# Optimization experiments

Measured on AMD Instinct MI355X. Metric: run time of the kernel, lower is better.

The kernel has to match this reference:

```python
import jax, jax.numpy as jnp
import numpy as np

B, F, D_IN, H, HEADS, NC = 2048, 64, 32, 128, 4, 16
EPG = 128            # random intra-graph edges per graph
N = B * F            # 131072 nodes
E = B * EPG          # 262144 edges (self-loops added in reference, like PyG GATConv)
LRELU_ATT = 0.2      # PyG GATConv negative_slope
LRELU_CLS = 0.01     # nn.LeakyReLU default


def setup_inputs() -> dict:
    key = jax.random.key(0)
    ks = jax.random.split(key, 24)
    emb = jax.random.normal(ks[0], (B, F, D_IN), jnp.float32)
    # per-graph random connectivity, offset so graphs are disjoint
    src_l = jax.random.randint(ks[1], (B, EPG), 0, F)
    tgt_l = jax.random.randint(ks[2], (B, EPG), 0, F)
    off = (jnp.arange(B) * F)[:, None]
    edge_index = jnp.stack([(src_l + off).reshape(-1), (tgt_l + off).reshape(-1)]).astype(jnp.int32)
    batch_idx = jnp.repeat(jnp.arange(B), F).astype(jnp.int32)
    s = 0.05
    return {
        'emb': emb, 'edge_index': edge_index, 'batch_idx': batch_idx,
        # fused aligner (single unique dim 32)
        'W_align': s * jax.random.normal(ks[3], (D_IN, H), jnp.float32),
        'b_align': jnp.zeros((H,), jnp.float32),
        'gate_logits': jnp.full((F,), 2.2, jnp.float32),
        # GATConv 1: in=H, out=H per head, heads=4, concat
        'W1': s * jax.random.normal(ks[4], (H, HEADS * H), jnp.float32),
        'a_src1': s * jax.random.normal(ks[5], (HEADS, H), jnp.float32),
        'a_dst1': s * jax.random.normal(ks[6], (HEADS, H), jnp.float32),
        'b1': jnp.zeros((HEADS * H,), jnp.float32),
        # GATConv 2: in=HEADS*H, out=H, heads=1, concat=False
        'W2': s * jax.random.normal(ks[7], (HEADS * H, H), jnp.float32),
        'a_src2': s * jax.random.normal(ks[8], (1, H), jnp.float32),
        'a_dst2': s * jax.random.normal(ks[9], (1, H), jnp.float32),
        'b2': jnp.zeros((H,), jnp.float32),
        # classifier MLP
        'Wc1': s * jax.random.normal(ks[10], (H, H // 2), jnp.float32),
        'bc1': jnp.zeros((H // 2,), jnp.float32),
        'Wc2': s * jax.random.normal(ks[11], (H // 2, NC), jnp.float32),
        'bc2': jnp.zeros((NC,), jnp.float32),
    }


def gat_layer(x, src, tgt, W, a_src, a_dst, b, concat):
    heads, dout = a_src.shape
    n = x.shape[0]
    h = (x @ W).reshape(n, heads, dout)                       # [N,h,d]
    e = jax.nn.leaky_relu(jnp.einsum('nhd,hd->nh', h, a_src)[src]
                          + jnp.einsum('nhd,hd->nh', h, a_dst)[tgt], LRELU_ATT)  # [E,h]
    m = jax.ops.segment_max(e, tgt, num_segments=n)           # segment softmax over in-neighbors
    p = jnp.exp(e - m[tgt])
    ssum = jax.ops.segment_sum(p, tgt, num_segments=n)
    alpha = p / (ssum[tgt] + 1e-16)
    out = jax.ops.segment_sum(h[src] * alpha[:, :, None], tgt, num_segments=n)
    out = out.reshape(n, heads * dout) if concat else out.mean(axis=1)
    return out + b


def reference(emb, edge_index, batch_idx, W_align, b_align, gate_logits,
              W1, a_src1, a_dst1, b1, W2, a_src2, a_dst2, b2, Wc1, bc1, Wc2, bc2):
    n = emb.shape[0] * emb.shape[1]
    aligned = emb @ W_align + b_align                         # fused align: [B,F,H]
    gate = jax.nn.sigmoid(gate_logits)                        # [F]
    x = (aligned * gate[None, :, None]).reshape(n, -1)        # gated node features [N,H]
    # add self-loops (GATConv default), eval mode -> dropout is identity
    loops = jnp.arange(n, dtype=edge_index.dtype)
    src = jnp.concatenate([edge_index[0], loops])
    tgt = jnp.concatenate([edge_index[1], loops])
    x = gat_layer(x, src, tgt, W1, a_src1, a_dst1, b1, True)  # [N, 4*H]
    x = jax.nn.elu(x)
    x = gat_layer(x, src, tgt, W2, a_src2, a_dst2, b2, False) # [N, H]
    gsum = jax.ops.segment_sum(x, batch_idx, num_segments=B)  # global_mean_pool
    cnt = jax.ops.segment_sum(jnp.ones((n, 1), x.dtype), batch_idx, num_segments=B)
    g = gsum / cnt                                            # [B, H]
    hc = jax.nn.leaky_relu(g @ Wc1 + bc1, LRELU_CLS)
    logits = hc @ Wc2 + bc2                                   # [B, NC]
    return logits, gate
```

## Files before the change

### kernel.cpp

```cpp
#include <hip/hip_runtime.h>
#include <math.h>

#define BLK 256

constexpr int Bg    = 2048;
constexpr int Fn    = 64;
constexpr int DIN   = 32;
constexpr int Hd    = 128;
constexpr int HEADS = 4;
constexpr int NC    = 16;
constexpr int EPG   = 128;
constexpr int Etot  = Bg * EPG;
constexpr int W1C   = HEADS * Hd;
constexpr int NSTR  = 68;
constexpr int EROW  = 132;
constexpr int PROW  = 68;
constexpr int NE    = EPG + Fn;

typedef __attribute__((ext_vector_type(8))) __bf16 bf16x8;
typedef __attribute__((ext_vector_type(4))) __bf16 bf16x4;
typedef __attribute__((ext_vector_type(4))) float  f32x4;

__device__ __align__(16) __bf16 g_wcombT[W1C * DIN];
__device__ float g_c1[W1C];
__device__ float g_c1s[16];
__device__ __align__(16) __bf16 g_w1F[HEADS*8*64*8];
__device__ __align__(16) __bf16 g_w2F[HEADS*4*8*64*8];
__device__ __align__(16) __bf16 g_wscF[HEADS*4*64*8];
__device__ __align__(16) __bf16 g_bs1F[64*8];

__global__ __launch_bounds__(BLK) void prep1(
    const float* __restrict__ Wa, const float* __restrict__ ba,
    const float* __restrict__ W1)
{
  __shared__ float WaS[DIN * Hd];
  const int tid = threadIdx.x;
  for (int i = tid; i < DIN * Hd; i += BLK) {
    int k = i >> 7, m = i & 127;
    WaS[m * DIN + k] = Wa[i];
  }
  __syncthreads();

  int i = blockIdx.x * BLK + tid;
  if (i < DIN * W1C) {
    int k = i & 31, n = i >> 5;
    float a0 = 0.f, a1 = 0.f, a2 = 0.f, a3 = 0.f;
    #pragma unroll
    for (int m = 0; m < Hd; m += 4) {
      a0 += WaS[(m  )*DIN + k] * W1[(m  )*W1C + n];
      a1 += WaS[(m+1)*DIN + k] * W1[(m+1)*W1C + n];
      a2 += WaS[(m+2)*DIN + k] * W1[(m+2)*W1C + n];
      a3 += WaS[(m+3)*DIN + k] * W1[(m+3)*W1C + n];
    }
    g_wcombT[i] = (__bf16)(a0 + a1 + a2 + a3);
  } else if (i < DIN*W1C + W1C) {
    int n = i - DIN*W1C;
    float a0 = 0.f, a1 = 0.f, a2 = 0.f, a3 = 0.f;
    #pragma unroll
    for (int m = 0; m < Hd; m += 4) {
      a0 += ba[m  ] * W1[(m  )*W1C + n];
      a1 += ba[m+1] * W1[(m+1)*W1C + n];
      a2 += ba[m+2] * W1[(m+2)*W1C + n];
      a3 += ba[m+3] * W1[(m+3)*W1C + n];
    }
    g_c1[n] = a0 + a1 + a2 + a3;
  }
}

constexpr int R_W2F  = 65536;
constexpr int R_W1F  = 16384;
constexpr int R_WSCZ = 8192;
constexpr int R_WSCD = 4096;
constexpr int R_BS1Z = 512;
constexpr int R_BS1D = 1024;
constexpr int R_C1S  = 128;
constexpr int B0 = R_W2F;
constexpr int B1 = B0 + R_W1F;
constexpr int B2 = B1 + R_WSCZ;
constexpr int B3 = B2 + R_WSCD;
constexpr int B4 = B3 + R_BS1Z;
constexpr int B5 = B4 + R_BS1D;
constexpr int P2_TOT = B5 + R_C1S;

__global__ __launch_bounds__(BLK) void prep2(
    const float* __restrict__ W2,
    const float* __restrict__ as1, const float* __restrict__ ad1,
    const float* __restrict__ as2, const float* __restrict__ ad2)
{
  int i = blockIdx.x * BLK + threadIdx.x;
  if (i < B0) {
    int k = i >> 7, n = i & 127;
    int hh = k >> 7, Ks = (k >> 5) & 3, q = (k >> 3) & 3, j = k & 7;
    int Nt = n >> 4, l = n & 15;
    int idx = (((hh*4 + Ks)*8 + Nt)*64 + (q*16 + l))*8 + j;
    g_w2F[idx] = (__bf16)W2[i];
  } else if (i < B1) {
    int j = i - B0;
    int jj = j & 7, lane = (j >> 3) & 63, T = j >> 9;
    int hh = T >> 3, Nt = T & 7;
    int q = lane >> 4, l = lane & 15;
    g_w1F[j] = g_wcombT[(hh*Hd + Nt*16 + l)*DIN + q*8 + jj];
  } else if (i < B2) {
    int j = i - B1;
    int lane = (j >> 3) & 63, c = lane & 15;
    if (c >= 2) g_wscF[j] = (__bf16)0.f;
  } else if (i < B3) {
    int j = i - B2;
    int p = j & 3, c = (j >> 2) & 1, k = j >> 3;
    const float* av = c ? ad2 : as2;
    float a0 = 0.f, a1 = 0.f, a2 = 0.f, a3 = 0.f;
    #pragma unroll
    for (int q = 0; q < 32; q += 4) {
      int f = p*32 + q;
      a0 += W2[(size_t)k*Hd + f    ] * av[f    ];
      a1 += W2[(size_t)k*Hd + f + 1] * av[f + 1];
      a2 += W2[(size_t)k*Hd + f + 2] * av[f + 2];
      a3 += W2[(size_t)k*Hd + f + 3] * av[f + 3];
    }
    float a = a0 + a1 + a2 + a3;
    a += __shfl_xor(a, 1);
    a += __shfl_xor(a, 2);
    if (p == 0) {
      int T = k >> 5, q2 = (k >> 3) & 3, jj = k & 7;
      g_wscF[(T*64 + q2*16 + c)*8 + jj] = (__bf16)a;
    }
  } else if (i < B4) {
    int j = i - B3;
    int lane = j >> 3, c = lane & 15;
    if (c >= 8) g_bs1F[j] = (__bf16)0.f;
  } else if (i < B5) {
    int j = i - B4;
    int p = j & 3, c = (j >> 2) & 7, kk = j >> 5;
    int h = c >> 1;
    const float* av = (c & 1) ? (ad1 + h*Hd) : (as1 + h*Hd);
    float a0 = 0.f, a1 = 0.f, a2 = 0.f, a3 = 0.f;
    #pragma unroll
    for (int q = 0; q < 32; q += 4) {
      int f = p*32 + q;
      a0 += (float)g_wcombT[(h*Hd + f    )*DIN + kk] * av[f    ];
      a1 += (float)g_wcombT[(h*Hd + f + 1)*DIN + kk] * av[f + 1];
      a2 += (float)g_wcombT[(h*Hd + f + 2)*DIN + kk] * av[f + 2];
      a3 += (float)g_wcombT[(h*Hd + f + 3)*DIN + kk] * av[f + 3];
    }
    float a = a0 + a1 + a2 + a3;
    a += __shfl_xor(a, 1);
    a += __shfl_xor(a, 2);
    if (p == 0) {
      int q2 = kk >> 3, jj = kk & 7;
      g_bs1F[(q2*16 + c)*8 + jj] = (__bf16)a;
    }
  } else if (i < P2_TOT) {
    int j = i - B5;
    int p = j & 7, c = j >> 3;
    float a = 0.f;
    if (c < 8) {
      int h = c >> 1;
      const float* av = (c & 1) ? (ad1 + h*Hd) : (as1 + h*Hd);
      #pragma unroll
      for (int q = 0; q < 16; ++q) {
        int f = p*16 + q;
        a += g_c1[h*Hd + f] * av[f];
      }
    }
    a += __shfl_xor(a, 1);
    a += __shfl_xor(a, 2);
    a += __shfl_xor(a, 4);
    if (p == 0) g_c1s[c] = a;
  }
}

#define SUMP(buf, t) ((float*)((char*)&Pbf[buf][(t)*PROW] + 128))
#define RCP(x) __builtin_amdgcn_rcpf(x)
__global__ __launch_bounds__(BLK, 3) void gat_main(
    const float* __restrict__ emb, const int* __restrict__ ei,
    const float* __restrict__ gate_logits,
    const float* __restrict__ b1, const float* __restrict__ b2,
    const float* __restrict__ Wc1, const float* __restrict__ bc1,
    const float* __restrict__ Wc2, const float* __restrict__ bc2,
    float* __restrict__ out)
{
  __shared__ __align__(16) __bf16 hT[Hd * NSTR];
  __shared__ __align__(16) __bf16 eluS[Fn * EROW];
  __shared__ __align__(16) __bf16 Pbf[2][Fn * PROW];
  __shared__ float sS1s[HEADS][Fn], sS1d[HEADS][Fn];

  unsigned* cells = (unsigned*)eluS;
  float*   gateS  = (float*)(eluS + 8192);
  float*   sSrc   = (float*)&Pbf[1][0];
  float*   sDst   = sSrc + Fn;
  __bf16*  wS     = (__bf16*)(sDst + Fn);
  float*   gpool  = (float*)(wS + Fn);
  float*   hcS    = gpool + Hd;

  const int b    = blockIdx.x;
  const int tid  = threadIdx.x;
  const int lane = tid & 63;
  const int wv   = tid >> 6;
  const int quad = lane >> 4;
  const int l15  = lane & 15;
  const int nodeBase = wv * 16;
  const int m0   = wv * 32;
  const int base = b * Fn;

  const f32x4 zero4 = {0.f, 0.f, 0.f, 0.f};

  int es = 0, et = 0, ecell = 0;
  if (tid < NE) {
    if (tid < EPG) {
      es = ei[(size_t)b*EPG + tid] - base;
      et = ei[(size_t)Etot + (size_t)b*EPG + tid] - base;
    } else {
      es = et = tid - EPG;
    }
    ecell = et * Fn + es;
  }
  {
    float4* c4 = (float4*)cells;
    const float4 z4 = {0.f,0.f,0.f,0.f};
    c4[tid] = z4; c4[tid + 256] = z4; c4[tid + 512] = z4; c4[tid + 768] = z4;
  }
  {
    float4* p4 = (float4*)&Pbf[0][0];
    const float4 z4 = {0.f,0.f,0.f,0.f};
    #pragma unroll
    for (int k = 0; k < 4; ++k) p4[tid + k*BLK] = z4;
    if (tid < 64) p4[1024 + tid] = z4;
  }
  if (tid < Fn) {
    float g = 1.f / (1.f + expf(-gate_logits[tid]));
    gateS[tid] = g;
    if (b == 0) out[Bg*NC + tid] = g;
  }
  float4 e0, e1;
  {
    const float* ar = emb + ((size_t)base + nodeBase + l15) * DIN + quad * 8;
    e0 = *(const float4*)ar;
    e1 = *(const float4*)(ar + 4);
  }
  __syncthreads();

  bool rep = false;
  if (tid < NE) rep = (atomicAdd(&cells[ecell], 1u) == 0u);

  float gq[4];
  #pragma unroll
  for (int r = 0; r < 4; ++r) gq[r] = gateS[nodeBase + quad*4 + r];

  bf16x8 Af;
  {
    const float gl = gateS[nodeBase + l15];
    Af[0]=(__bf16)(e0.x*gl); Af[1]=(__bf16)(e0.y*gl); Af[2]=(__bf16)(e0.z*gl); Af[3]=(__bf16)(e0.w*gl);
    Af[4]=(__bf16)(e1.x*gl); Af[5]=(__bf16)(e1.y*gl); Af[6]=(__bf16)(e1.z*gl); Af[7]=(__bf16)(e1.w*gl);
  }
  {
    bf16x8 Bs = *(const bf16x8*)(g_bs1F + lane*8);
    f32x4 ds = __builtin_amdgcn_mfma_f32_16x16x32_bf16(Af, Bs, zero4, 0, 0, 0);
    if (l15 < 8) {
      const float cc = g_c1s[l15];
      const int h = l15 >> 1;
      float* dstArr = (l15 & 1) ? &sS1d[h][0] : &sS1s[h][0];
      #pragma unroll
      for (int r = 0; r < 4; ++r) {
        int m = nodeBase + quad*4 + r;
        dstArr[m] = ds[r] + gq[r] * cc;
      }
    }
  }
  #pragma unroll
  for (int Nt = 0; Nt < 8; ++Nt) {
    const int n = Nt*16 + l15;
    bf16x8 Bf = *(const bf16x8*)(g_w1F + ((0*8 + Nt)*64 + lane)*8);
    f32x4 d = __builtin_amdgcn_mfma_f32_16x16x32_bf16(Af, Bf, zero4, 0, 0, 0);
    const float c1v = g_c1[0*Hd + n];
    bf16x4 hw;
    #pragma unroll
    for (int r = 0; r < 4; ++r) hw[r] = (__bf16)(d[r] + c1v * gq[r]);
    *(bf16x4*)(hT + n*NSTR + nodeBase + quad*4) = hw;
  }
  __syncthreads();

  float fm = 0.f;
  if (tid < NE && rep) {
    fm = (float)cells[ecell];
    float e = sS1s[0][es] + sS1d[0][et];
    e = (e > 0.f) ? e : 0.2f * e;
    float pe = fm * __expf(e);
    Pbf[0][et*PROW + es] = (__bf16)pe;
    atomicAdd(SUMP(0, et), pe);
  }
  __syncthreads();

  f32x4 acc[8];
  #pragma unroll
  for (int i = 0; i < 8; ++i) acc[i] = zero4;
  f32x4 accS = zero4;

  #pragma unroll 1
  for (int hh = 0; hh < HEADS; ++hh) {
    const int cur = hh & 1;
    {
      bf16x8 Ac[2][2];
      #pragma unroll
      for (int Mi = 0; Mi < 2; ++Mi)
        #pragma unroll
        for (int Ks = 0; Ks < 2; ++Ks)
          Ac[Mi][Ks] = *(const bf16x8*)(hT + (m0 + Mi*16 + l15)*NSTR + Ks*32 + quad*8);
      float4 b1v[2];
      #pragma unroll
      for (int Mi = 0; Mi < 2; ++Mi)
        b1v[Mi] = *(const float4*)&b1[hh*Hd + m0 + Mi*16 + quad*4];
      #pragma unroll
      for (int Nt = 0; Nt < 4; ++Nt) {
        bf16x8 B0f = *(const bf16x8*)(Pbf[cur] + (Nt*16 + l15)*PROW + quad*8);
        bf16x8 B1f = *(const bf16x8*)(Pbf[cur] + (Nt*16 + l15)*PROW + 32 + quad*8);
        const int t = Nt*16 + l15;
        const float si = RCP(*SUMP(cur, t) + 1e-16f);
        #pragma unroll
        for (int Mi = 0; Mi < 2; ++Mi) {
          f32x4 d = __builtin_amdgcn_mfma_f32_16x16x32_bf16(Ac[Mi][0], B0f, zero4, 0, 0, 0);
          d = __builtin_amdgcn_mfma_f32_16x16x32_bf16(Ac[Mi][1], B1f, d, 0, 0, 0);
          bf16x4 w;
          #pragma unroll
          for (int r = 0; r < 4; ++r) {
            float hv = d[r]*si + b1v[Mi][r];
            hv = (hv > 0.f) ? hv : (__expf(hv) - 1.f);
            w[r] = (__bf16)hv;
          }
          *(bf16x4*)(eluS + t*EROW + m0 + Mi*16 + quad*4) = w;
        }
      }
    }
    if (hh >= 1) {
      float4* p4 = (float4*)&Pbf[(hh+1)&1][0];
      const float4 z4 = {0.f,0.f,0.f,0.f};
      p4[tid] = z4; p4[tid + 256] = z4;
      if (tid < 32) p4[tid + 512] = z4;
    }
    __syncthreads();

    #pragma unroll
    for (int Ks = 0; Ks < 4; ++Ks) {
      bf16x8 A2 = *(const bf16x8*)(eluS + (nodeBase + l15)*EROW + Ks*32 + quad*8);
      #pragma unroll
      for (int Nt = 0; Nt < 8; ++Nt) {
        bf16x8 B2 = *(const bf16x8*)(g_w2F + (((hh*4 + Ks)*8 + Nt)*64 + lane)*8);
        acc[Nt] = __builtin_amdgcn_mfma_f32_16x16x32_bf16(A2, B2, acc[Nt], 0, 0, 0);
      }
      bf16x8 Bs2 = *(const bf16x8*)(g_wscF + ((hh*4 + Ks)*64 + lane)*8);
      accS = __builtin_amdgcn_mfma_f32_16x16x32_bf16(A2, Bs2, accS, 0, 0, 0);
    }
    if (hh < 3) {
      #pragma unroll
      for (int Nt = 0; Nt < 8; ++Nt) {
        const int n = Nt*16 + l15;
        bf16x8 Bf = *(const bf16x8*)(g_w1F + (((hh+1)*8 + Nt)*64 + lane)*8);
        f32x4 d = __builtin_amdgcn_mfma_f32_16x16x32_bf16(Af, Bf, zero4, 0, 0, 0);
        const float c1v = g_c1[(hh+1)*Hd + n];
        bf16x4 hw;
        #pragma unroll
        for (int r = 0; r < 4; ++r) hw[r] = (__bf16)(d[r] + c1v * gq[r]);
        *(bf16x4*)(hT + n*NSTR + nodeBase + quad*4) = hw;
      }
      if (tid < NE && rep) {
        float e = sS1s[hh+1][es] + sS1d[hh+1][et];
        e = (e > 0.f) ? e : 0.2f * e;
        float pe = fm * __expf(e);
        Pbf[(hh+1)&1][et*PROW + es] = (__bf16)pe;
        atomicAdd(SUMP((hh+1)&1, et), pe);
      }
    } else {
      #pragma unroll
      for (int Nt = 0; Nt < 8; ++Nt) {
        const int n = Nt*16 + l15;
        bf16x4 hw;
        #pragma unroll
        for (int r = 0; r < 4; ++r) hw[r] = (__bf16)acc[Nt][r];
        *(bf16x4*)(hT + n*NSTR + nodeBase + quad*4) = hw;
      }
      if (l15 == 0) {
        #pragma unroll
        for (int r = 0; r < 4; ++r) sSrc[nodeBase + quad*4 + r] = accS[r];
      } else if (l15 == 1) {
        #pragma unroll
        for (int r = 0; r < 4; ++r) sDst[nodeBase + quad*4 + r] = accS[r];
      }
    }
    __syncthreads();
  }

  if (tid < NE && rep) {
    float e = sSrc[es] + sDst[et];
    e = (e > 0.f) ? e : 0.2f * e;
    float pe = fm * __expf(e);
    Pbf[0][et*PROW + es] = (__bf16)pe;
    atomicAdd(SUMP(0, et), pe);
  }
  __syncthreads();

  {
    const int s_ = tid >> 2, part = tid & 3;
    float a = 0.f;
    #pragma unroll
    for (int q = 0; q < 16; ++q) {
      const int t = part*16 + q;
      a += RCP(*SUMP(0, t) + 1e-16f) * (float)Pbf[0][t*PROW + s_];
    }
    a += __shfl_xor(a, 1);
    a += __shfl_xor(a, 2);
    if (part == 0) wS[s_] = (__bf16)(a * (1.f/64.f));
  }
  __syncthreads();

  {
    #pragma unroll
    for (int Mi = 0; Mi < 2; ++Mi) {
      f32x4 d = zero4;
      #pragma unroll
      for (int Ks = 0; Ks < 2; ++Ks) {
        bf16x8 A = *(const bf16x8*)(hT + (m0 + Mi*16 + l15)*NSTR + Ks*32 + quad*8);
        bf16x8 Bw = *(const bf16x8*)(wS + Ks*32 + quad*8);
        d = __builtin_amdgcn_mfma_f32_16x16x32_bf16(A, Bw, d, 0, 0, 0);
      }
      if (l15 == 0) {
        #pragma unroll
        for (int r = 0; r < 4; ++r) {
          const int f = m0 + Mi*16 + quad*4 + r;
          gpool[f] = d[r] + b2[f];
        }
      }
    }
  }
  __syncthreads();

  {
    const int c = tid >> 2, p = tid & 3;
    float a = 0.f;
    #pragma unroll
    for (int i = 0; i < 32; ++i) {
      const int k = p*32 + i;
      a += gpool[k] * Wc1[k*Fn + c];
    }
    a += __shfl_xor(a, 1);
    a += __shfl_xor(a, 2);
    if (p == 0) {
      a += bc1[c];
      hcS[c] = (a > 0.f) ? a : 0.01f * a;
    }
  }
  __syncthreads();

  {
    const int c = tid >> 4, p = tid & 15;
    float a = 0.f;
    #pragma unroll
    for (int i = 0; i < 4; ++i) {
      const int k = p*4 + i;
      a += hcS[k] * Wc2[k*NC + c];
    }
    a += __shfl_xor(a, 1);
    a += __shfl_xor(a, 2);
    a += __shfl_xor(a, 4);
    a += __shfl_xor(a, 8);
    if (p == 0) out[b*NC + c] = a + bc2[c];
  }
}
#undef SUMP
#undef RCP

extern "C" void kernel_launch(void* const* d_in, const int* in_sizes, int n_in,
                              void* d_out, int out_size, void* d_ws, size_t ws_size,
                              hipStream_t stream) {
  const float* emb = (const float*)d_in[0];
  const int*   ei  = (const int*)  d_in[1];
  const float* Wa  = (const float*)d_in[3];
  const float* ba  = (const float*)d_in[4];
  const float* gl  = (const float*)d_in[5];
  const float* W1  = (const float*)d_in[6];
  const float* as1 = (const float*)d_in[7];
  const float* ad1 = (const float*)d_in[8];
  const float* b1  = (const float*)d_in[9];
  const float* W2  = (const float*)d_in[10];
  const float* as2 = (const float*)d_in[11];
  const float* ad2 = (const float*)d_in[12];
  const float* b2  = (const float*)d_in[13];
  const float* Wc1 = (const float*)d_in[14];
  const float* bc1 = (const float*)d_in[15];
  const float* Wc2 = (const float*)d_in[16];
  const float* bc2 = (const float*)d_in[17];
  float* out = (float*)d_out;

  const int prep1N = DIN*W1C + W1C;
  hipLaunchKernelGGL(prep1, dim3((prep1N + BLK - 1)/BLK), dim3(BLK), 0, stream,
                     Wa, ba, W1);
  hipLaunchKernelGGL(prep2, dim3((P2_TOT + BLK - 1)/BLK), dim3(BLK), 0, stream,
                     W2, as1, ad1, as2, ad2);
  hipLaunchKernelGGL(gat_main, dim3(Bg), dim3(BLK), 0, stream,
                     emb, ei, gl, b1, b2, Wc1, bc1, Wc2, bc2, out);
}
```

Baseline: 189.7 us.

## Double block size to eight waves and split feature tiles across wave halves

The main kernel now launches 512-thread blocks. Each of the four node groups is handled by two waves, and those two waves split the output-feature N tiles of the W1 and W2 matmuls between them. The aggregation M tiles and the pooling and classifier reductions are redistributed over all eight waves. The goal is more waves per CU and shorter per-wave serial MFMA chains under the same per-block LDS footprint. The trade-offs are duplicated emb loads, extra shuffle steps, and an aggressive launch-bounds hint that may cap registers and cause spills.

```diff
diff --git a/kernel.cpp b/kernel.cpp
--- a/kernel.cpp
+++ b/kernel.cpp
@@ -2,6 +2,7 @@
 #include <math.h>
 
 #define BLK 256
+#define MBLK 512
 
 constexpr int Bg    = 2048;
 constexpr int Fn    = 64;
@@ -171,7 +172,7 @@
 
 #define SUMP(buf, t) ((float*)((char*)&Pbf[buf][(t)*PROW] + 128))
 #define RCP(x) __builtin_amdgcn_rcpf(x)
-__global__ __launch_bounds__(BLK, 3) void gat_main(
+__global__ __launch_bounds__(MBLK, 6) void gat_main(
     const float* __restrict__ emb, const int* __restrict__ ei,
     const float* __restrict__ gate_logits,
     const float* __restrict__ b1, const float* __restrict__ b2,
@@ -196,10 +197,12 @@
   const int tid  = threadIdx.x;
   const int lane = tid & 63;
   const int wv   = tid >> 6;
+  const int ng   = wv & 3;
+  const int nh   = wv >> 2;
   const int quad = lane >> 4;
   const int l15  = lane & 15;
-  const int nodeBase = wv * 16;
-  const int m0   = wv * 32;
+  const int nodeBase = ng * 16;
+  const int m0   = wv * 16;
   const int base = b * Fn;
 
   const f32x4 zero4 = {0.f, 0.f, 0.f, 0.f};
@@ -217,13 +220,12 @@
   {
     float4* c4 = (float4*)cells;
     const float4 z4 = {0.f,0.f,0.f,0.f};
-    c4[tid] = z4; c4[tid + 256] = z4; c4[tid + 512] = z4; c4[tid + 768] = z4;
+    c4[tid] = z4; c4[tid + 512] = z4;
   }
   {
     float4* p4 = (float4*)&Pbf[0][0];
     const float4 z4 = {0.f,0.f,0.f,0.f};
-    #pragma unroll
-    for (int k = 0; k < 4; ++k) p4[tid + k*BLK] = z4;
+    p4[tid] = z4; p4[tid + 512] = z4;
     if (tid < 64) p4[1024 + tid] = z4;
   }
   if (tid < Fn) {
@@ -252,7 +254,7 @@
     Af[0]=(__bf16)(e0.x*gl); Af[1]=(__bf16)(e0.y*gl); Af[2]=(__bf16)(e0.z*gl); Af[3]=(__bf16)(e0.w*gl);
     Af[4]=(__bf16)(e1.x*gl); Af[5]=(__bf16)(e1.y*gl); Af[6]=(__bf16)(e1.z*gl); Af[7]=(__bf16)(e1.w*gl);
   }
-  {
+  if (nh == 0) {
     bf16x8 Bs = *(const bf16x8*)(g_bs1F + lane*8);
     f32x4 ds = __builtin_amdgcn_mfma_f32_16x16x32_bf16(Af, Bs, zero4, 0, 0, 0);
     if (l15 < 8) {
@@ -267,9 +269,10 @@
     }
   }
   #pragma unroll
-  for (int Nt = 0; Nt < 8; ++Nt) {
-    const int n = Nt*16 + l15;
-    bf16x8 Bf = *(const bf16x8*)(g_w1F + ((0*8 + Nt)*64 + lane)*8);
+  for (int Nt = 0; Nt < 4; ++Nt) {
+    const int Ntg = nh*4 + Nt;
+    const int n = Ntg*16 + l15;
+    bf16x8 Bf = *(const bf16x8*)(g_w1F + ((0*8 + Ntg)*64 + lane)*8);
     f32x4 d = __builtin_amdgcn_mfma_f32_16x16x32_bf16(Af, Bf, zero4, 0, 0, 0);
     const float c1v = g_c1[0*Hd + n];
     bf16x4 hw;
@@ -290,51 +293,43 @@
   }
   __syncthreads();
 
-  f32x4 acc[8];
+  f32x4 acc[4];
   #pragma unroll
-  for (int i = 0; i < 8; ++i) acc[i] = zero4;
+  for (int i = 0; i < 4; ++i) acc[i] = zero4;
   f32x4 accS = zero4;
 
   #pragma unroll 1
   for (int hh = 0; hh < HEADS; ++hh) {
     const int cur = hh & 1;
     {
-      bf16x8 Ac[2][2];
-      #pragma unroll
-      for (int Mi = 0; Mi < 2; ++Mi)
-        #pragma unroll
-        for (int Ks = 0; Ks < 2; ++Ks)
-          Ac[Mi][Ks] = *(const bf16x8*)(hT + (m0 + Mi*16 + l15)*NSTR + Ks*32 + quad*8);
-      float4 b1v[2];
-      #pragma unroll
-      for (int Mi = 0; Mi < 2; ++Mi)
-        b1v[Mi] = *(const float4*)&b1[hh*Hd + m0 + Mi*16 + quad*4];
+      bf16x8 Ac[2];
+      #pragma unroll
+      for (int Ks = 0; Ks < 2; ++Ks)
+        Ac[Ks] = *(const bf16x8*)(hT + (m0 + l15)*NSTR + Ks*32 + quad*8);
+      float4 b1v = *(const float4*)&b1[hh*Hd + m0 + quad*4];
       #pragma unroll
       for (int Nt = 0; Nt < 4; ++Nt) {
         bf16x8 B0f = *(const bf16x8*)(Pbf[cur] + (Nt*16 + l15)*PROW + quad*8);
         bf16x8 B1f = *(const bf16x8*)(Pbf[cur] + (Nt*16 + l15)*PROW + 32 + quad*8);
         const int t = Nt*16 + l15;
         const float si = RCP(*SUMP(cur, t) + 1e-16f);
+        f32x4 d = __builtin_amdgcn_mfma_f32_16x16x32_bf16(Ac[0], B0f, zero4, 0, 0, 0);
+        d = __builtin_amdgcn_mfma_f32_16x16x32_bf16(Ac[1], B1f, d, 0, 0, 0);
+        bf16x4 w;
         #pragma unroll
-        for (int Mi = 0; Mi < 2; ++Mi) {
-          f32x4 d = __builtin_amdgcn_mfma_f32_16x16x32_bf16(Ac[Mi][0], B0f, zero4, 0, 0, 0);
-          d = __builtin_amdgcn_mfma_f32_16x16x32_bf16(Ac[Mi][1], B1f, d, 0, 0, 0);
-          bf16x4 w;
-          #pragma unroll
-          for (int r = 0; r < 4; ++r) {
-            float hv = d[r]*si + b1v[Mi][r];
-            hv = (hv > 0.f) ? hv : (__expf(hv) - 1.f);
-            w[r] = (__bf16)hv;
-          }
-          *(bf16x4*)(eluS + t*EROW + m0 + Mi*16 + quad*4) = w;
+        for (int r = 0; r < 4; ++r) {
+          float hv = d[r]*si + b1v[r];
+          hv = (hv > 0.f) ? hv : (__expf(hv) - 1.f);
+          w[r] = (__bf16)hv;
         }
+        *(bf16x4*)(eluS + t*EROW + m0 + quad*4) = w;
       }
     }
     if (hh >= 1) {
       float4* p4 = (float4*)&Pbf[(hh+1)&1][0];
       const float4 z4 = {0.f,0.f,0.f,0.f};
-      p4[tid] = z4; p4[tid + 256] = z4;
-      if (tid < 32) p4[tid + 512] = z4;
+      p4[tid] = z4;
+      if (tid < 32) p4[512 + tid] = z4;
     }
     __syncthreads();
 
@@ -342,18 +337,22 @@
     for (int Ks = 0; Ks < 4; ++Ks) {
       bf16x8 A2 = *(const bf16x8*)(eluS + (nodeBase + l15)*EROW + Ks*32 + quad*8);
       #pragma unroll
-      for (int Nt = 0; Nt < 8; ++Nt) {
-        bf16x8 B2 = *(const bf16x8*)(g_w2F + (((hh*4 + Ks)*8 + Nt)*64 + lane)*8);
+      for (int Nt = 0; Nt < 4; ++Nt) {
+        const int Ntg = nh*4 + Nt;
+        bf16x8 B2 = *(const bf16x8*)(g_w2F + (((hh*4 + Ks)*8 + Ntg)*64 + lane)*8);
         acc[Nt] = __builtin_amdgcn_mfma_f32_16x16x32_bf16(A2, B2, acc[Nt], 0, 0, 0);
       }
-      bf16x8 Bs2 = *(const bf16x8*)(g_wscF + ((hh*4 + Ks)*64 + lane)*8);
-      accS = __builtin_amdgcn_mfma_f32_16x16x32_bf16(A2, Bs2, accS, 0, 0, 0);
+      if (nh == 0) {
+        bf16x8 Bs2 = *(const bf16x8*)(g_wscF + ((hh*4 + Ks)*64 + lane)*8);
+        accS = __builtin_amdgcn_mfma_f32_16x16x32_bf16(A2, Bs2, accS, 0, 0, 0);
+      }
     }
     if (hh < 3) {
       #pragma unroll
-      for (int Nt = 0; Nt < 8; ++Nt) {
-        const int n = Nt*16 + l15;
-        bf16x8 Bf = *(const bf16x8*)(g_w1F + (((hh+1)*8 + Nt)*64 + lane)*8);
+      for (int Nt = 0; Nt < 4; ++Nt) {
+        const int Ntg = nh*4 + Nt;
+        const int n = Ntg*16 + l15;
+        bf16x8 Bf = *(const bf16x8*)(g_w1F + (((hh+1)*8 + Ntg)*64 + lane)*8);
         f32x4 d = __builtin_amdgcn_mfma_f32_16x16x32_bf16(Af, Bf, zero4, 0, 0, 0);
         const float c1v = g_c1[(hh+1)*Hd + n];
         bf16x4 hw;
@@ -370,19 +369,21 @@
       }
     } else {
       #pragma unroll
-      for (int Nt = 0; Nt < 8; ++Nt) {
-        const int n = Nt*16 + l15;
+      for (int Nt = 0; Nt < 4; ++Nt) {
+        const int n = (nh*4 + Nt)*16 + l15;
         bf16x4 hw;
         #pragma unroll
         for (int r = 0; r < 4; ++r) hw[r] = (__bf16)acc[Nt][r];
         *(bf16x4*)(hT + n*NSTR + nodeBase + quad*4) = hw;
       }
-      if (l15 == 0) {
-        #pragma unroll
-        for (int r = 0; r < 4; ++r) sSrc[nodeBase + quad*4 + r] = accS[r];
-      } else if (l15 == 1) {
-        #pragma unroll
-        for (int r = 0; r < 4; ++r) sDst[nodeBase + quad*4 + r] = accS[r];
+      if (nh == 0) {
+        if (l15 == 0) {
+          #pragma unroll
+          for (int r = 0; r < 4; ++r) sSrc[nodeBase + quad*4 + r] = accS[r];
+        } else if (l15 == 1) {
+          #pragma unroll
+          for (int r = 0; r < 4; ++r) sDst[nodeBase + quad*4 + r] = accS[r];
+        }
       }
     }
     __syncthreads();
@@ -398,50 +399,49 @@
   __syncthreads();
 
   {
-    const int s_ = tid >> 2, part = tid & 3;
+    const int s_ = tid >> 3, part = tid & 7;
     float a = 0.f;
     #pragma unroll
-    for (int q = 0; q < 16; ++q) {
-      const int t = part*16 + q;
+    for (int q = 0; q < 8; ++q) {
+      const int t = part*8 + q;
       a += RCP(*SUMP(0, t) + 1e-16f) * (float)Pbf[0][t*PROW + s_];
     }
     a += __shfl_xor(a, 1);
     a += __shfl_xor(a, 2);
+    a += __shfl_xor(a, 4);
     if (part == 0) wS[s_] = (__bf16)(a * (1.f/64.f));
   }
   __syncthreads();
 
   {
-    #pragma unroll
-    for (int Mi = 0; Mi < 2; ++Mi) {
-      f32x4 d = zero4;
-      #pragma unroll
-      for (int Ks = 0; Ks < 2; ++Ks) {
-        bf16x8 A = *(const bf16x8*)(hT + (m0 + Mi*16 + l15)*NSTR + Ks*32 + quad*8);
-        bf16x8 Bw = *(const bf16x8*)(wS + Ks*32 + quad*8);
-        d = __builtin_amdgcn_mfma_f32_16x16x32_bf16(A, Bw, d, 0, 0, 0);
-      }
-      if (l15 == 0) {
-        #pragma unroll
-        for (int r = 0; r < 4; ++r) {
-          const int f = m0 + Mi*16 + quad*4 + r;
-          gpool[f] = d[r] + b2[f];
-        }
-      }
-    }
-  }
-  __syncthreads();
-
-  {
-    const int c = tid >> 2, p = tid & 3;
+    f32x4 d = zero4;
+    #pragma unroll
+    for (int Ks = 0; Ks < 2; ++Ks) {
+      bf16x8 A = *(const bf16x8*)(hT + (m0 + l15)*NSTR + Ks*32 + quad*8);
+      bf16x8 Bw = *(const bf16x8*)(wS + Ks*32 + quad*8);
+      d = __builtin_amdgcn_mfma_f32_16x16x32_bf16(A, Bw, d, 0, 0, 0);
+    }
+    if (l15 == 0) {
+      #pragma unroll
+      for (int r = 0; r < 4; ++r) {
+        const int f = m0 + quad*4 + r;
+        gpool[f] = d[r] + b2[f];
+      }
+    }
+  }
+  __syncthreads();
+
+  {
+    const int c = tid >> 3, p = tid & 7;
     float a = 0.f;
     #pragma unroll
-    for (int i = 0; i < 32; ++i) {
-      const int k = p*32 + i;
+    for (int i = 0; i < 16; ++i) {
+      const int k = p*16 + i;
       a += gpool[k] * Wc1[k*Fn + c];
     }
     a += __shfl_xor(a, 1);
     a += __shfl_xor(a, 2);
+    a += __shfl_xor(a, 4);
     if (p == 0) {
       a += bc1[c];
       hcS[c] = (a > 0.f) ? a : 0.01f * a;
@@ -450,17 +450,18 @@
   __syncthreads();
 
   {
-    const int c = tid >> 4, p = tid & 15;
+    const int c = tid >> 5, p = tid & 31;
     float a = 0.f;
     #pragma unroll
-    for (int i = 0; i < 4; ++i) {
-      const int k = p*4 + i;
+    for (int i = 0; i < 2; ++i) {
+      const int k = p*2 + i;
       a += hcS[k] * Wc2[k*NC + c];
     }
     a += __shfl_xor(a, 1);
     a += __shfl_xor(a, 2);
     a += __shfl_xor(a, 4);
     a += __shfl_xor(a, 8);
+    a += __shfl_xor(a, 16);
     if (p == 0) out[b*NC + c] = a + bc2[c];
   }
 }
@@ -494,6 +495,6 @@
                      Wa, ba, W1);
   hipLaunchKernelGGL(prep2, dim3((P2_TOT + BLK - 1)/BLK), dim3(BLK), 0, stream,
                      W2, as1, ad1, as2, ad2);
-  hipLaunchKernelGGL(gat_main, dim3(Bg), dim3(BLK), 0, stream,
+  hipLaunchKernelGGL(gat_main, dim3(Bg), dim3(MBLK), 0, stream,
                      emb, ei, gl, b1, b2, Wc1, bc1, Wc2, bc2, out);
 }
```

Result: slower. 294.0 us (+55.0%).
